# Kernel optimization log

Measured on AMD Instinct MI355X. Metric: run time of the kernel, lower is better.

## Reference

```python
import jax, jax.numpy as jnp
import numpy as np

B, N, E, EH, IB, DF, HID, P, TOPK, NE = 16, 978, 512, 512, 64, 2304, 512, 8, 50, 50000
SKIP = 0.2          # args.graph_skip_conn
NEG_INF = -1e20     # markoff value for non-top-k entries before softmax
LN_EPS = 1e-5


def setup_inputs() -> dict:
    key = jax.random.key(0)
    ks = jax.random.split(key, 20)
    g = lambda i, shape, s=0.05: jax.random.normal(ks[i], shape, dtype=jnp.float32) * s
    return dict(
        x1=jax.random.normal(ks[0], (B, N), dtype=jnp.float32),
        drug1=jax.random.normal(ks[1], (B, DF), dtype=jnp.float32),
        drug2=jax.random.normal(ks[2], (B, DF), dtype=jnp.float32),
        eps=jax.random.normal(ks[3], (B, IB), dtype=jnp.float32),
        edge_index=jax.random.randint(ks[4], (2, NE), 0, N),
        gate_W=g(5, (1, E)), gate_b=jnp.zeros((E,), jnp.float32),
        emb=g(6, (N, E), 1.0),
        encW1=g(7, (E, EH)), encb1=jnp.zeros((EH,), jnp.float32),
        encW2=g(8, (EH, 2 * IB)), encb2=jnp.zeros((2 * IB,), jnp.float32),
        netW1=g(9, (DF, E)), netb1=jnp.zeros((E,), jnp.float32),
        netW2=g(10, (E, 2 * IB)), netb2=jnp.zeros((2 * IB,), jnp.float32),
        ln_g=jnp.ones((2 * IB,), jnp.float32), ln_b=jnp.zeros((2 * IB,), jnp.float32),
        feat_mask=g(11, (4 * IB,), 1.0),
        W_sims=g(12, (P, 4 * IB, HID)),
        gcnW1=g(13, (2 * IB, HID)), gcnb1=jnp.zeros((HID,), jnp.float32),
        gcnW2=g(14, (HID, 2 * IB)), gcnb2=jnp.zeros((2 * IB,), jnp.float32),
        decW1=g(15, (IB, EH)), decb1=jnp.zeros((EH,), jnp.float32),
        bn_g=jnp.ones((EH,), jnp.float32), bn_b=jnp.zeros((EH,), jnp.float32),
        decW2=g(16, (EH, N)), decb2=jnp.zeros((N,), jnp.float32),
    )


def _forward(x1, drug1, drug2, eps, edge_index,
             gate_W, gate_b, emb, encW1, encb1, encW2, encb2,
             netW1, netb1, netW2, netb2, ln_g, ln_b,
             feat_mask, W_sims, gcnW1, gcnb1, gcnW2, gcnb2,
             decW1, decb1, bn_g, bn_b, decW2, decb2):
    # --- Encoder_x1: per-gene gated embedding -> MLP -> [B,N,2*IB] ---
    gate = jax.nn.sigmoid(x1[..., None] @ gate_W + gate_b)          # [B,N,E]
    h = gate * emb[None]                                            # [B,N,E]
    h = jax.nn.gelu(h @ encW1 + encb1, approximate=False)
    H = h @ encW2 + encb2                                           # [B,N,128]

    # --- drug feature net: Linear-ReLU-Linear-LayerNorm -> [B,128] ---
    def drug_embed(d):
        t = jax.nn.relu(d @ netW1 + netb1)
        t = t @ netW2 + netb2
        mu = t.mean(-1, keepdims=True)
        var = t.var(-1, keepdims=True)
        return (t - mu) * jax.lax.rsqrt(var + LN_EPS) * ln_g + ln_b

    D1 = drug_embed(drug1)
    D2 = drug_embed(drug2)
    fus1 = jnp.concatenate([H, jnp.broadcast_to(D1[:, None, :], (B, N, 2 * IB))], -1)  # [B,N,256]
    fus2 = jnp.concatenate([H, jnp.broadcast_to(D2[:, None, :], (B, N, 2 * IB))], -1)

    # --- init adjacency from edge_index (to_dense_adj), shared across batch ---
    init_adj = jnp.zeros((N, N), jnp.float32).at[edge_index[0], edge_index[1]].set(1.0)

    # --- attention-metric graph learner with feature denoise + kNN sparsify ---
    def learn_adj(fus):
        feats = fus * jax.nn.sigmoid(feat_mask)                      # feature mask
        hp = jax.nn.relu(jnp.einsum('bnd,pdh->bpnh', feats, W_sims)) # [B,P,N,HID]
        att = jnp.einsum('bpnh,bpmh->bnm', hp, hp) / P               # [B,N,N] (mean over perspectives)

        def sparsify(a):  # per-sample kNN mask + row softmax
            vals, idx = jax.lax.top_k(a, TOPK)
            out = jnp.full_like(a, NEG_INF).at[jnp.arange(N)[:, None], idx].set(vals)
            return jax.nn.softmax(out, axis=-1)

        adj = jax.vmap(sparsify)(att)
        return SKIP * init_adj[None] + (1.0 - SKIP) * adj

    adj1 = learn_adj(fus1)
    adj2 = learn_adj(fus2)

    # --- 2-layer GCN on learned graph (symmetric norm, self loops, edge weights) ---
    eye = jnp.eye(N, dtype=jnp.float32)

    def gcn_layer(x, adj, W, b):
        ahat = adj + eye[None]
        deg = ahat.sum(-2)                                           # in-degree by target (PyG flow)
        dinv = jax.lax.rsqrt(deg)
        norm = ahat * dinv[:, :, None] * dinv[:, None, :]            # [B,N,N]
        return jnp.einsum('bji,bjf->bif', norm, x @ W) + b

    t = jax.nn.relu(gcn_layer(H, adj1, gcnW1, gcnb1))
    node = gcn_layer(t, adj1, gcnW2, gcnb2)                          # [B,N,128]

    # --- global mean pool + VIB reparametrization ---
    gemb = node.mean(1)                                              # [B,128]
    mu = gemb[:, :IB]
    std = jax.nn.softplus(gemb[:, IB:] - IB)
    z = mu + eps * std                                               # [B,64]

    # --- decoder_x2: Linear-BatchNorm-ReLU-Linear-ReLU ---
    d = z @ decW1 + decb1
    bm = d.mean(0)
    bv = d.var(0)
    d = (d - bm) * jax.lax.rsqrt(bv + LN_EPS) * bn_g + bn_b
    d = jax.nn.relu(d)
    x2_pred = jax.nn.relu(d @ decW2 + decb2)                         # [B,N]
    return x2_pred, adj2, mu, std


def reference(x1, drug1, drug2, eps, edge_index,
              gate_W, gate_b, emb, encW1, encb1, encW2, encb2,
              netW1, netb1, netW2, netb2, ln_g, ln_b,
              feat_mask, W_sims, gcnW1, gcnb1, gcnW2, gcnb2,
              decW1, decb1, bn_g, bn_b, decW2, decb2):
    return _forward(x1, drug1, drug2, eps, edge_index,
                    gate_W, gate_b, emb, encW1, encb1, encW2, encb2,
                    netW1, netb1, netW2, netb2, ln_g, ln_b,
                    feat_mask, W_sims, gcnW1, gcnb1, gcnW2, gcnb2,
                    decW1, decb1, bn_g, bn_b, decW2, decb2)
```

## Files before the change

kernel.cpp:

```cpp
#include <hip/hip_runtime.h>
#include <cmath>

namespace {

constexpr int B = 16;
constexpr int N = 978;
constexpr int M = B * N;
constexpr int IB2 = 128;
constexpr int KATT = 4096;
constexpr int KCH = 1024;
constexpr int NCH = KATT / KCH;
constexpr int DF = 2304;
constexpr int TOPKK = 50;
constexpr int NEDGE = 50000;
constexpr int CANDMAX = 64;
constexpr int WST = 120;
constexpr int JQ = 245;

typedef __attribute__((ext_vector_type(8))) short bf16x8;
typedef __attribute__((ext_vector_type(4))) float f32x4;

__device__ __forceinline__ float geluf(float x) {
  return 0.5f * x * (1.f + erff(x * 0.7071067811865476f));
}
__device__ __forceinline__ float sigm(float x) { return 1.f / (1.f + expf(-x)); }
__device__ __forceinline__ double sigm64(double x) { return 1.0 / (1.0 + exp(-x)); }

__device__ __forceinline__ unsigned short f2bf(float f) {
  union { float f; unsigned u; } x; x.f = f;
  unsigned r = (x.u + 0x7FFFu + ((x.u >> 16) & 1u)) >> 16;
  return (unsigned short)r;
}
__device__ __forceinline__ float bf2f(unsigned short s) {
  union { float f; unsigned u; } x; x.u = ((unsigned)s) << 16; return x.f;
}

__global__ void k_wt(const float* __restrict__ wsims, const float* __restrict__ fm,
                     unsigned short* __restrict__ wth, unsigned short* __restrict__ wtl) {
  int t = blockIdx.x * 256 + threadIdx.x;
  int n = t >> 8, k = t & 255;
  int p = n >> 9, h = n & 511;
  double v = (double)wsims[(size_t)p * 131072 + (size_t)k * 512 + h] * sigm64((double)fm[k]);
  float vf = (float)v;
  unsigned short hi = f2bf(vf);
  wth[t] = hi;
  wtl[t] = f2bf(vf - bf2f(hi));
}

__global__ void k_wtrans(const float* __restrict__ W, unsigned short* __restrict__ TH,
                         unsigned short* __restrict__ TL, int K, int Nc) {
  int t = blockIdx.x * 256 + threadIdx.x;
  if (t >= K * Nc) return;
  int n = t / K, k = t - n * K;
  float v = W[(size_t)k * Nc + n];
  unsigned short hi = f2bf(v);
  TH[t] = hi;
  TL[t] = f2bf(v - bf2f(hi));
}

__global__ void k_fus(const float* __restrict__ Hb, const float* __restrict__ DD,
                      unsigned short* __restrict__ fh, unsigned short* __restrict__ fl) {
  int t = blockIdx.x * 256 + threadIdx.x;
  int k = t & 255;
  int row = t >> 8;
  int b = row / N;
  float v = (k < 128) ? Hb[(size_t)row * 128 + k] : DD[(size_t)b * 128 + (k - 128)];
  unsigned short hi = f2bf(v);
  fh[t] = hi;
  fl[t] = f2bf(v - bf2f(hi));
}

__global__ void k_gate_emb_bf(const float* __restrict__ x1, const float* __restrict__ gW,
                              const float* __restrict__ gb, const float* __restrict__ emb,
                              unsigned short* __restrict__ GH, unsigned short* __restrict__ GL) {
  size_t t = (size_t)blockIdx.x * 256 + threadIdx.x;
  int e = (int)(t & 511);
  size_t bn = t >> 9;
  int n = (int)(bn % N);
  float g = sigm(x1[bn] * gW[e] + gb[e]);
  float v = g * emb[(size_t)n * 512 + e];
  unsigned short hi = f2bf(v);
  GH[t] = hi;
  GL[t] = f2bf(v - bf2f(hi));
}

__global__ void k_zero(float* __restrict__ p, int n) {
  int t = blockIdx.x * 256 + threadIdx.x;
  if (t < n) p[t] = 0.f;
}

__global__ void k_scatter(const int* __restrict__ ei, float* __restrict__ adj) {
  int t = blockIdx.x * 256 + threadIdx.x;
  if (t < NEDGE) {
    int r = ei[t], c = ei[NEDGE + t];
    adj[(size_t)r * N + c] = 1.f;
  }
}

__device__ __forceinline__ void stage_tile(const unsigned short* __restrict__ gbase, int grow0,
                                           int rowmax, int k0, int ldk, char* lds, int tid) {
#pragma unroll
  for (int it = 0; it < 2; it++) {
    int r = (tid >> 2) + it * 64;
    int c8 = tid & 3;
    int gr = grow0 + r;
    uint4 v = make_uint4(0u, 0u, 0u, 0u);
    if (gr < rowmax) v = *reinterpret_cast<const uint4*>(&gbase[(size_t)gr * ldk + k0 + c8 * 8]);
    int off = (r * 64 + c8 * 16) ^ ((r & 7) << 4);
    *reinterpret_cast<uint4*>(lds + off) = v;
  }
}

__device__ __forceinline__ bf16x8 frag(const char* lds, int r, int k8) {
  int off = (r * 64 + k8 * 16) ^ ((r & 7) << 4);
  return *reinterpret_cast<const bf16x8*>(lds + off);
}

template <int ACT, bool HASBIAS, bool OUTF32, bool OUTBF>
__global__ __launch_bounds__(256) void k_mgemm(const unsigned short* __restrict__ AH,
                                               const unsigned short* __restrict__ AL,
                                               const unsigned short* __restrict__ BTH,
                                               const unsigned short* __restrict__ BTL,
                                               const float* __restrict__ bias,
                                               float* __restrict__ Cf,
                                               unsigned short* __restrict__ CbH,
                                               unsigned short* __restrict__ CbL,
                                               int Mm, int K, int Nc) {
  __shared__ __align__(16) char Ah[8192];
  __shared__ __align__(16) char Al[8192];
  __shared__ __align__(16) char Bh[8192];
  __shared__ __align__(16) char Bl[8192];
  const int m0 = blockIdx.x * 128;
  const int n0 = blockIdx.y * 128;
  const int tid = threadIdx.x;
  const int wave = tid >> 6, lane = tid & 63;
  f32x4 acc[2][8];
#pragma unroll
  for (int i = 0; i < 2; i++)
#pragma unroll
    for (int j = 0; j < 8; j++) acc[i][j] = (f32x4){0.f, 0.f, 0.f, 0.f};

  for (int k0 = 0; k0 < K; k0 += 32) {
    stage_tile(AH, m0, Mm, k0, K, Ah, tid);
    stage_tile(AL, m0, Mm, k0, K, Al, tid);
    stage_tile(BTH, n0, Nc, k0, K, Bh, tid);
    stage_tile(BTL, n0, Nc, k0, K, Bl, tid);
    __syncthreads();
    bf16x8 ah[2], al[2];
#pragma unroll
    for (int rf = 0; rf < 2; rf++) {
      int r = wave * 32 + rf * 16 + (lane & 15);
      ah[rf] = frag(Ah, r, lane >> 4);
      al[rf] = frag(Al, r, lane >> 4);
    }
#pragma unroll
    for (int cf = 0; cf < 8; cf++) {
      int rB = cf * 16 + (lane & 15);
      bf16x8 bh = frag(Bh, rB, lane >> 4);
      bf16x8 bl = frag(Bl, rB, lane >> 4);
#pragma unroll
      for (int rf = 0; rf < 2; rf++) {
        acc[rf][cf] = __builtin_amdgcn_mfma_f32_16x16x32_bf16(ah[rf], bh, acc[rf][cf], 0, 0, 0);
        acc[rf][cf] = __builtin_amdgcn_mfma_f32_16x16x32_bf16(ah[rf], bl, acc[rf][cf], 0, 0, 0);
        acc[rf][cf] = __builtin_amdgcn_mfma_f32_16x16x32_bf16(al[rf], bh, acc[rf][cf], 0, 0, 0);
      }
    }
    __syncthreads();
  }
#pragma unroll
  for (int rf = 0; rf < 2; rf++)
#pragma unroll
    for (int cf = 0; cf < 8; cf++)
#pragma unroll
      for (int r4 = 0; r4 < 4; r4++) {
        int row = m0 + wave * 32 + rf * 16 + ((lane >> 4) << 2) + r4;
        int col = n0 + cf * 16 + (lane & 15);
        if (row < Mm) {
          float v = acc[rf][cf][r4];
          if (HASBIAS) v += bias[col];
          if (ACT == 1) v = geluf(v);
          if (ACT == 2) v = fmaxf(v, 0.f);
          size_t idx = (size_t)row * Nc + col;
          if (OUTF32) Cf[idx] = v;
          if (OUTBF) {
            unsigned short hi = f2bf(v);
            CbH[idx] = hi;
            CbL[idx] = f2bf(v - bf2f(hi));
          }
        }
      }
}

__global__ __launch_bounds__(256) void k_hp_mma(const unsigned short* __restrict__ FH,
                                                const unsigned short* __restrict__ FL,
                                                const unsigned short* __restrict__ WTHc,
                                                const unsigned short* __restrict__ WTLc,
                                                float* __restrict__ CH) {
  __shared__ __align__(16) char Ah[8192];
  __shared__ __align__(16) char Al[8192];
  __shared__ __align__(16) char Bh[8192];
  __shared__ __align__(16) char Bl[8192];
  const int m0 = blockIdx.x * 128;
  const int n0 = blockIdx.y * 128;
  const int tid = threadIdx.x;
  const int wave = tid >> 6, lane = tid & 63;
  f32x4 acc[2][8];
#pragma unroll
  for (int i = 0; i < 2; i++)
#pragma unroll
    for (int j = 0; j < 8; j++) acc[i][j] = (f32x4){0.f, 0.f, 0.f, 0.f};

  for (int k0 = 0; k0 < 256; k0 += 32) {
    stage_tile(FH, m0, M, k0, 256, Ah, tid);
    stage_tile(FL, m0, M, k0, 256, Al, tid);
    stage_tile(WTHc, n0, KCH, k0, 256, Bh, tid);
    stage_tile(WTLc, n0, KCH, k0, 256, Bl, tid);
    __syncthreads();
    bf16x8 ah[2], al[2];
#pragma unroll
    for (int rf = 0; rf < 2; rf++) {
      int r = wave * 32 + rf * 16 + (lane & 15);
      ah[rf] = frag(Ah, r, lane >> 4);
      al[rf] = frag(Al, r, lane >> 4);
    }
#pragma unroll
    for (int cf = 0; cf < 8; cf++) {
      int rB = cf * 16 + (lane & 15);
      bf16x8 bh = frag(Bh, rB, lane >> 4);
      bf16x8 bl = frag(Bl, rB, lane >> 4);
#pragma unroll
      for (int rf = 0; rf < 2; rf++) {
        acc[rf][cf] = __builtin_amdgcn_mfma_f32_16x16x32_bf16(ah[rf], bh, acc[rf][cf], 0, 0, 0);
        acc[rf][cf] = __builtin_amdgcn_mfma_f32_16x16x32_bf16(ah[rf], bl, acc[rf][cf], 0, 0, 0);
        acc[rf][cf] = __builtin_amdgcn_mfma_f32_16x16x32_bf16(al[rf], bh, acc[rf][cf], 0, 0, 0);
      }
    }
    __syncthreads();
  }
#pragma unroll
  for (int rf = 0; rf < 2; rf++)
#pragma unroll
    for (int cf = 0; cf < 8; cf++)
#pragma unroll
      for (int r4 = 0; r4 < 4; r4++) {
        int row = m0 + wave * 32 + rf * 16 + ((lane >> 4) << 2) + r4;
        int col = n0 + cf * 16 + (lane & 15);
        if (row < M) CH[(size_t)row * KCH + col] = fmaxf(acc[rf][cf][r4], 0.f);
      }
}

__global__ __launch_bounds__(256) void k_mu(const float* __restrict__ CH, float* __restrict__ MU) {
  __shared__ double red[8][33];
  int b = blockIdx.y, jg = blockIdx.x;
  int jloc = threadIdx.x & 31, s = threadIdx.x >> 5;
  int j = jg * 32 + jloc;
  const float* p = CH + (size_t)b * N * KCH + j;
  double acc = 0.0;
  for (int n = s; n < N; n += 8) acc += (double)p[(size_t)n * KCH];
  red[s][jloc] = acc;
  __syncthreads();
  if (s == 0) {
    double t = 0.0;
#pragma unroll
    for (int k = 0; k < 8; k++) t += red[k][jloc];
    MU[b * KCH + j] = (float)(t * (1.0 / (double)N));
  }
}

__global__ __launch_bounds__(256) void k_centerq(const float* __restrict__ CH,
                                                 const float* __restrict__ MU,
                                                 unsigned short* __restrict__ CHB,
                                                 double* __restrict__ qv) {
  int r = blockIdx.x * 4 + (threadIdx.x >> 6);
  int lane = threadIdx.x & 63;
  int b = r / N;
  const float* row = CH + (size_t)r * KCH;
  const float* mu = MU + (size_t)b * KCH;
  double q = 0.0;
#pragma unroll
  for (int jp = 0; jp < 2; jp++) {
    int j0 = lane * 8 + jp * 512;
    float4 v0 = *reinterpret_cast<const float4*>(&row[j0]);
    float4 v1 = *reinterpret_cast<const float4*>(&row[j0 + 4]);
    float4 m0 = *reinterpret_cast<const float4*>(&mu[j0]);
    float4 m1 = *reinterpret_cast<const float4*>(&mu[j0 + 4]);
    unsigned short cb[8];
    cb[0] = f2bf(v0.x - m0.x); cb[1] = f2bf(v0.y - m0.y);
    cb[2] = f2bf(v0.z - m0.z); cb[3] = f2bf(v0.w - m0.w);
    cb[4] = f2bf(v1.x - m1.x); cb[5] = f2bf(v1.y - m1.y);
    cb[6] = f2bf(v1.z - m1.z); cb[7] = f2bf(v1.w - m1.w);
    *reinterpret_cast<uint4*>(&CHB[(size_t)r * KCH + j0]) = *reinterpret_cast<uint4*>(cb);
    q += (double)m0.x * v0.x + (double)m0.y * v0.y + (double)m0.z * v0.z + (double)m0.w * v0.w
       + (double)m1.x * v1.x + (double)m1.y * v1.y + (double)m1.z * v1.z + (double)m1.w * v1.w;
  }
  for (int off = 32; off > 0; off >>= 1) q += __shfl_down(q, off);
  if (lane == 0) qv[r] += q;
}

template <bool ACC>
__global__ __launch_bounds__(256) void k_syrk_mma(const unsigned short* __restrict__ CHB,
                                                  float* __restrict__ ATT) {
  __shared__ __align__(16) char At[8192];
  __shared__ __align__(16) char Bt[8192];
  const int T = 8;
  int pr = blockIdx.x;
  int ti = 0, rem = pr;
  while (rem >= T - ti) { rem -= T - ti; ti++; }
  int tj = ti + rem;
  int b = blockIdx.y;
  const unsigned short* base = CHB + (size_t)b * N * KCH;
  const int tid = threadIdx.x;
  const int wave = tid >> 6, lane = tid & 63;
  f32x4 acc[2][8];
#pragma unroll
  for (int i = 0; i < 2; i++)
#pragma unroll
    for (int j = 0; j < 8; j++) acc[i][j] = (f32x4){0.f, 0.f, 0.f, 0.f};

  for (int k0 = 0; k0 < KCH; k0 += 32) {
    stage_tile(base, ti * 128, N, k0, KCH, At, tid);
    stage_tile(base, tj * 128, N, k0, KCH, Bt, tid);
    __syncthreads();
    bf16x8 af[2];
#pragma unroll
    for (int rf = 0; rf < 2; rf++)
      af[rf] = frag(At, wave * 32 + rf * 16 + (lane & 15), lane >> 4);
#pragma unroll
    for (int cf = 0; cf < 8; cf++) {
      bf16x8 bf_ = frag(Bt, cf * 16 + (lane & 15), lane >> 4);
#pragma unroll
      for (int rf = 0; rf < 2; rf++)
        acc[rf][cf] = __builtin_amdgcn_mfma_f32_16x16x32_bf16(af[rf], bf_, acc[rf][cf], 0, 0, 0);
    }
    __syncthreads();
  }
  float* att = ATT + (size_t)b * N * N;
#pragma unroll
  for (int rf = 0; rf < 2; rf++)
#pragma unroll
    for (int cf = 0; cf < 8; cf++)
#pragma unroll
      for (int r4 = 0; r4 < 4; r4++) {
        int row = ti * 128 + wave * 32 + rf * 16 + ((lane >> 4) << 2) + r4;
        int col = tj * 128 + cf * 16 + (lane & 15);
        if (row < N && col < N) {
          float v = acc[rf][cf][r4];
          if (ACC) {
            att[(size_t)row * N + col] += v;
            if (ti != tj) att[(size_t)col * N + row] += v;
          } else {
            att[(size_t)row * N + col] = v;
            if (ti != tj) att[(size_t)col * N + row] = v;
          }
        }
      }
}

__global__ __launch_bounds__(256) void k_topk(float* __restrict__ ATT, const double* __restrict__ qv,
                                              const float* __restrict__ INITA,
                                              int* __restrict__ fcnt, int* __restrict__ frow,
                                              int* __restrict__ fcw, int* __restrict__ fidx,
                                              float* __restrict__ fv32) {
  int row = blockIdx.x;
  int n = row % N;
  int b = row / N;
  float* arow = ATT + (size_t)row * N;
  __shared__ unsigned keys[1024];
  __shared__ float svs[1024];
  __shared__ float outr[N];
  __shared__ float sred;
  __shared__ int s_slot, s_cw;
  int tid = threadIdx.x;
  double qn = qv[row];
  unsigned kreg[4];
#pragma unroll
  for (int c = 0; c < 4; c++) {
    int i = tid + 256 * c;
    unsigned kk = 0xFFFFFFFFu;
    float sv = -1e30f;
    if (i < N) {
      sv = (float)((double)arow[i] + qv[(size_t)b * N + i] - qn);
      unsigned u = __float_as_uint(sv);
      u ^= (u >> 31) ? 0xFFFFFFFFu : 0x80000000u;
      kk = ((~u) & 0xFFFFFC00u) | (unsigned)i;
    }
    svs[i] = sv;
    kreg[c] = kk;
  }
  __syncthreads();
  for (int ksz = 2; ksz <= 1024; ksz <<= 1) {
    for (int j = ksz >> 1; j > 0; j >>= 1) {
      if (j <= 32) {
#pragma unroll
        for (int c = 0; c < 4; c++) {
          int e = tid + 256 * c;
          unsigned pk = __shfl_xor(kreg[c], j);
          bool takemin = (((e & j) == 0) == ((e & ksz) == 0));
          unsigned mn = kreg[c] < pk ? kreg[c] : pk;
          unsigned mx = kreg[c] < pk ? pk : kreg[c];
          kreg[c] = takemin ? mn : mx;
        }
      } else if (j >= 256) {
        int sw = j >> 8;
#pragma unroll
        for (int c = 0; c < 4; c++) {
          if ((c & sw) == 0) {
            int e = tid + 256 * c;
            bool up = (e & ksz) == 0;
            unsigned a = kreg[c], b2 = kreg[c | sw];
            if ((a > b2) == up) { kreg[c] = b2; kreg[c | sw] = a; }
          }
        }
      } else {
#pragma unroll
        for (int c = 0; c < 4; c++) keys[tid + 256 * c] = kreg[c];
        __syncthreads();
#pragma unroll
        for (int c = 0; c < 4; c++) {
          int e = tid + 256 * c;
          unsigned pk = keys[e ^ j];
          bool takemin = (((e & j) == 0) == ((e & ksz) == 0));
          unsigned mn = kreg[c] < pk ? kreg[c] : pk;
          unsigned mx = kreg[c] < pk ? pk : kreg[c];
          kreg[c] = takemin ? mn : mx;
        }
        __syncthreads();
      }
    }
  }
#pragma unroll
  for (int c = 0; c < 4; c++) keys[tid + 256 * c] = kreg[c];
  __syncthreads();

  float v49 = svs[keys[49] & 1023u];
  float v50v = svs[keys[50] & 1023u];
  float FLAGW = 8e-3f + 2e-5f * fabsf(v49);
  bool flag = (v50v >= v49 - FLAGW);
  if (flag) {
    if (tid == 0) {
      int cin = 0;
      for (int r = 0; r < 50; r++)
        if (svs[keys[r] & 1023u] > v49 + FLAGW) cin++;
      int rhi = 50;
      while (rhi < 113) {
        float vv = svs[keys[rhi + 1] & 1023u];
        if (vv >= v49 - FLAGW) rhi++; else break;
      }
      int w = rhi - cin + 1;
      if (w > CANDMAX) w = CANDMAX;
      if (cin + w < 50) w = 50 - cin;
      int slot = atomicAdd(fcnt, 1);
      frow[slot] = row;
      fcw[slot] = cin | (w << 8);
      s_slot = slot;
      s_cw = cin | (w << 8);
    }
    __syncthreads();
    int slot = s_slot;
    int tot = (s_cw & 255) + (s_cw >> 8);
    for (int r = tid; r < tot; r += 256) {
      unsigned kk = keys[r];
      fidx[(size_t)slot * WST + r] = (int)(kk & 1023u);
      fv32[(size_t)slot * WST + r] = svs[kk & 1023u];
    }
    __syncthreads();
  }

  float vmax = svs[keys[0] & 1023u];
  float e = 0.f;
  int myidx = 0;
  if (tid < TOPKK) {
    unsigned kk = keys[tid];
    myidx = (int)(kk & 1023u);
    e = expf((svs[myidx] - vmax) * 0.125f);
  }
  float s = e;
  for (int off = 32; off > 0; off >>= 1) s += __shfl_down(s, off);
  if (tid == 0) sred = s;
  for (int m2 = tid; m2 < N; m2 += 256) outr[m2] = 0.2f * INITA[(size_t)n * N + m2];
  __syncthreads();
  if (tid < TOPKK) outr[myidx] = 0.2f * INITA[(size_t)n * N + myidx] + 0.8f * (e / sred);
  __syncthreads();
  for (int m2 = tid; m2 < N; m2 += 256) arow[m2] = outr[m2];
}

__global__ __launch_bounds__(256) void k_fixup(float* __restrict__ ATT, const float* __restrict__ INITA,
                                               const int* __restrict__ fcnt, const int* __restrict__ frow,
                                               const int* __restrict__ fcw, const int* __restrict__ fidx,
                                               const float* __restrict__ fv32) {
  __shared__ double wts[56];
  __shared__ int mm[56];
  __shared__ int s_tot;
  int tid = threadIdx.x;
  int cnt = *fcnt;
  for (int slot = blockIdx.x; slot < cnt; slot += gridDim.x) {
    int row = frow[slot];
    int cw = fcw[slot];
    int cin = cw & 255, w = cw >> 8;
    int n = row % N;
    __syncthreads();
    if (tid == 0) {
      int need = 50 - cin;
      if (need > w) need = w;
      double cv[CANDMAX]; int cm[CANDMAX]; float cs[CANDMAX];
      for (int c = 0; c < w; c++) {
        float sv = fv32[(size_t)slot * WST + cin + c];
        cv[c] = (double)sv * 0.125;
        cm[c] = fidx[(size_t)slot * WST + cin + c];
        cs[c] = sv;
      }
      int ord[CANDMAX];
      for (int c = 0; c < w; c++) ord[c] = c;
      for (int a2 = 0; a2 < w; a2++) {
        int best = a2;
        for (int c2 = a2 + 1; c2 < w; c2++) {
          int i1 = ord[c2], i0 = ord[best];
          if (cv[i1] > cv[i0] || (cv[i1] == cv[i0] && cm[i1] < cm[i0])) best = c2;
        }
        int tswap = ord[a2]; ord[a2] = ord[best]; ord[best] = tswap;
      }
      double b_in = cv[ord[need - 1]];
      double b_out = (need < w) ? cv[ord[need]] : -1e300;
      const double DATT = 1e-3;
      double fac[56];
      int tot = 0;
      for (int r = 0; r < cin; r++) {
        wts[tot] = (double)fv32[(size_t)slot * WST + r];
        mm[tot] = fidx[(size_t)slot * WST + r];
        fac[tot++] = 1.0;
      }
      if (need == w || b_in - b_out > DATT) {
        for (int t3 = 0; t3 < need; t3++) {
          wts[tot] = (double)cs[ord[t3]];
          mm[tot] = cm[ord[t3]];
          fac[tot++] = 1.0;
        }
      } else {
        int gs = 0;
        while (gs < w && cv[ord[gs]] > b_in + DATT) gs++;
        int ge = w - 1;
        while (ge >= 0 && cv[ord[ge]] < b_out - DATT) ge--;
        double mid = 0.5 * (b_in + b_out);
        while (ge - gs + 1 > 3) {
          if (cv[ord[gs]] - mid >= mid - cv[ord[ge]]) gs++;
          else ge--;
        }
        int fullc = gs;
        int gcount = ge - gs + 1;
        int gneed = need - fullc;
        if (gneed < 0) gneed = 0;
        if (gneed > gcount) gneed = gcount;
        double frac = (gcount > 0) ? (double)gneed / (double)gcount : 0.0;
        for (int t3 = 0; t3 < fullc; t3++) {
          wts[tot] = (double)cs[ord[t3]];
          mm[tot] = cm[ord[t3]];
          fac[tot++] = 1.0;
        }
        for (int t3 = gs; t3 <= ge; t3++) {
          wts[tot] = (double)cs[ord[t3]];
          mm[tot] = cm[ord[t3]];
          fac[tot++] = frac;
        }
      }
      double vmax = -1e300;
      for (int r = 0; r < tot; r++)
        if (fac[r] > 0.0 && wts[r] > vmax) vmax = wts[r];
      double S = 0.0;
      for (int r = 0; r < tot; r++) {
        double e = fac[r] * exp((wts[r] - vmax) * 0.125);
        wts[r] = e;
        S += e;
      }
      double inv = 1.0 / S;
      for (int r = 0; r < tot; r++) wts[r] *= inv;
      s_tot = tot;
    }
    __syncthreads();
    int tot = s_tot;
    float* arow = ATT + (size_t)row * N;
    for (int m2 = tid; m2 < N; m2 += 256) arow[m2] = 0.2f * INITA[(size_t)n * N + m2];
    __syncthreads();
    if (tid < tot && wts[tid] > 0.0)
      arow[mm[tid]] = 0.2f * INITA[(size_t)n * N + mm[tid]] + 0.8f * (float)wts[tid];
    __syncthreads();
  }
}

__global__ __launch_bounds__(256) void k_degp(const float* __restrict__ ADJ, float* __restrict__ DPART) {
  int ch = blockIdx.x, b = blockIdx.y;
  int tid = threadIdx.x;
  float reg[4] = {0.f, 0.f, 0.f, 0.f};
  int j0 = ch * 123, j1 = j0 + 123;
  if (j1 > N) j1 = N;
  const float* adj = ADJ + (size_t)b * N * N;
  for (int j = j0; j < j1; j++) {
    const float* rowp = adj + (size_t)j * N;
#pragma unroll
    for (int k = 0; k < 4; k++) {
      int i = tid + 256 * k;
      if (i < N) reg[k] += rowp[i];
    }
  }
  float* dp = DPART + ((size_t)b * 8 + ch) * N;
#pragma unroll
  for (int k = 0; k < 4; k++) {
    int i = tid + 256 * k;
    if (i < N) dp[i] = reg[k];
  }
}
__global__ void k_degf(const float* __restrict__ DPART, float* __restrict__ DINV) {
  int t = blockIdx.x * 256 + threadIdx.x;
  if (t >= M) return;
  int b = t / N, i = t - b * N;
  float s = 1.f;
#pragma unroll
  for (int c = 0; c < 8; c++) s += DPART[((size_t)b * 8 + c) * N + i];
  DINV[t] = rsqrtf(s);
}

__global__ __launch_bounds__(256) void k_spmmp(const float* __restrict__ ADJ, const float* __restrict__ DINV,
                                               const float* __restrict__ X, float* __restrict__ PP) {
  __shared__ float As[16][132];
  __shared__ float Ws[16][132];
  const int tid = threadIdx.x;
  const int i0 = blockIdx.x * 128;
  const int b = blockIdx.z >> 2;
  const int q = blockIdx.z & 3;
  const int jstart = q * JQ;
  const int jend = (q == 3) ? N : (jstart + JQ);
  const float* adj = ADJ + (size_t)b * N * N;
  const float* dv = DINV + b * N;
  const float* xb = X + (size_t)b * N * 128;
  const int ty = tid >> 4, tx = tid & 15;
  float acc[8][8];
#pragma unroll
  for (int i = 0; i < 8; i++)
#pragma unroll
    for (int j = 0; j < 8; j++) acc[i][j] = 0.f;

  for (int j0 = jstart; j0 < jend; j0 += 16) {
#pragma unroll
    for (int l = 0; l < 8; l++) {
      int idx = tid + l * 256;
      int r = idx >> 7, c = idx & 127;
      int j = j0 + r, i = i0 + c;
      float v = 0.f;
      if (j < jend && i < N) {
        float dj = dv[j];
        v = adj[(size_t)j * N + i] * dj;
        if (i == j) v += dj;
      }
      As[r][c] = v;
      float w = 0.f;
      if (j < jend) w = xb[(size_t)j * 128 + c];
      Ws[r][c] = w;
    }
    __syncthreads();
#pragma unroll
    for (int k = 0; k < 16; k++) {
      float a[8], bb[8];
      *reinterpret_cast<float4*>(&a[0]) = *reinterpret_cast<const float4*>(&As[k][ty * 8]);
      *reinterpret_cast<float4*>(&a[4]) = *reinterpret_cast<const float4*>(&As[k][ty * 8 + 4]);
      *reinterpret_cast<float4*>(&bb[0]) = *reinterpret_cast<const float4*>(&Ws[k][tx * 8]);
      *reinterpret_cast<float4*>(&bb[4]) = *reinterpret_cast<const float4*>(&Ws[k][tx * 8 + 4]);
#pragma unroll
      for (int i = 0; i < 8; i++)
#pragma unroll
        for (int j = 0; j < 8; j++) acc[i][j] = fmaf(a[i], bb[j], acc[i][j]);
    }
    __syncthreads();
  }
#pragma unroll
  for (int i = 0; i < 8; i++) {
    int row = i0 + ty * 8 + i;
    if (row >= N) continue;
#pragma unroll
    for (int j4 = 0; j4 < 2; j4++) {
      float4 v;
      float* vv = reinterpret_cast<float*>(&v);
#pragma unroll
      for (int j = 0; j < 4; j++) vv[j] = acc[i][j4 * 4 + j];
      *reinterpret_cast<float4*>(&PP[(((size_t)q * M) + (size_t)b * N + row) * 128 +
                                     tx * 8 + j4 * 4]) = v;
    }
  }
}

template <bool HASBIAS, bool OUTBF>
__global__ void k_spmmc(const float* __restrict__ PP, const float* __restrict__ DINV,
                        const float* __restrict__ bias, float* __restrict__ OUT,
                        unsigned short* __restrict__ OH, unsigned short* __restrict__ OL) {
  int t = blockIdx.x * 256 + threadIdx.x;
  int row = t >> 7, f = t & 127;
  float v = ((PP[t] + PP[(size_t)M * 128 + t]) +
             (PP[(size_t)2 * M * 128 + t] + PP[(size_t)3 * M * 128 + t])) * DINV[row];
  if (HASBIAS) v += bias[f];
  if (OUTBF) {
    unsigned short hi = f2bf(v);
    OH[t] = hi;
    OL[t] = f2bf(v - bf2f(hi));
  } else {
    OUT[t] = v;
  }
}

__global__ __launch_bounds__(256) void k_drug_l1(const float* __restrict__ d1, const float* __restrict__ d2,
                                                 const float* __restrict__ W, const float* __restrict__ bias,
                                                 float* __restrict__ T1) {
  __shared__ float row[DF];
  int blk = blockIdx.x;
  const float* dr = ((blk & 16) ? d2 : d1) + (size_t)(blk & 15) * DF;
  for (int i = threadIdx.x; i < DF; i += 256) row[i] = dr[i];
  __syncthreads();
  for (int e = threadIdx.x; e < 512; e += 256) {
    float s = bias[e];
    for (int k = 0; k < DF; k++) s = fmaf(row[k], W[(size_t)k * 512 + e], s);
    T1[(size_t)blk * 512 + e] = fmaxf(s, 0.f);
  }
}

__global__ __launch_bounds__(128) void k_drug_l2(const float* __restrict__ T1, const float* __restrict__ W,
                                                 const float* __restrict__ bias, const float* __restrict__ lg,
                                                 const float* __restrict__ lb, float* __restrict__ D) {
  __shared__ float row[512];
  __shared__ float red[4];
  int blk = blockIdx.x;
  int e = threadIdx.x;
  for (int i = e; i < 512; i += 128) row[i] = T1[(size_t)blk * 512 + i];
  __syncthreads();
  float s = bias[e];
  for (int k = 0; k < 512; k++) s = fmaf(row[k], W[k * 128 + e], s);
  float t = s;
  for (int off = 32; off > 0; off >>= 1) t += __shfl_down(t, off);
  if ((e & 63) == 0) red[e >> 6] = t;
  __syncthreads();
  float mean = (red[0] + red[1]) * (1.f / 128.f);
  float dd = s - mean;
  float wv = dd * dd;
  for (int off = 32; off > 0; off >>= 1) wv += __shfl_down(wv, off);
  if ((e & 63) == 0) red[2 + (e >> 6)] = wv;
  __syncthreads();
  float var = (red[2] + red[3]) * (1.f / 128.f);
  D[(size_t)blk * 128 + e] = dd * rsqrtf(var + 1e-5f) * lg[e] + lb[e];
}

__global__ void k_gemb(const float* __restrict__ NODE, float* __restrict__ GEMB) {
  int t = blockIdx.x * 256 + threadIdx.x;
  int b = t >> 7, f = t & 127;
  const float* p = NODE + (size_t)b * N * IB2 + f;
  float s = 0.f;
  for (int n2 = 0; n2 < N; n2++) s += p[(size_t)n2 * IB2];
  GEMB[t] = s * (1.f / (float)N);
}

__global__ void k_heads(const float* __restrict__ GEMB, const float* __restrict__ EPS,
                        float* __restrict__ out_mu, float* __restrict__ out_std, float* __restrict__ Z) {
  int t = blockIdx.x * 256 + threadIdx.x;
  int b = t >> 6, q = t & 63;
  float mu = GEMB[b * 128 + q];
  float xs = GEMB[b * 128 + 64 + q] - 64.f;
  float sp = (xs > 20.f) ? xs : log1pf(expf(xs));
  out_mu[t] = mu;
  out_std[t] = sp;
  Z[t] = mu + EPS[t] * sp;
}

__global__ __launch_bounds__(512) void k_dec1(const float* __restrict__ Z, const float* __restrict__ W1,
                                              const float* __restrict__ b1, const float* __restrict__ bg,
                                              const float* __restrict__ bb, float* __restrict__ DEC) {
  int f = threadIdx.x;
  float d[16];
  for (int b = 0; b < 16; b++) {
    float s = b1[f];
    for (int k = 0; k < 64; k++) s = fmaf(Z[b * 64 + k], W1[k * 512 + f], s);
    d[b] = s;
  }
  float m = 0.f;
  for (int b = 0; b < 16; b++) m += d[b];
  m *= (1.f / 16.f);
  float v = 0.f;
  for (int b = 0; b < 16; b++) { float t = d[b] - m; v += t * t; }
  v *= (1.f / 16.f);
  float sc = rsqrtf(v + 1e-5f) * bg[f];
  float sh = bb[f];
  for (int b = 0; b < 16; b++) {
    float x = (d[b] - m) * sc + sh;
    DEC[b * 512 + f] = fmaxf(x, 0.f);
  }
}

__global__ void k_dec2(const float* __restrict__ DEC, const float* __restrict__ W2,
                       const float* __restrict__ b2, float* __restrict__ X2) {
  int t = blockIdx.x * 256 + threadIdx.x;
  if (t >= M) return;
  int b = t / N, n2 = t - b * N;
  float s = b2[n2];
  const float* db = DEC + b * 512;
  for (int f = 0; f < 512; f++) s = fmaf(db[f], W2[(size_t)f * N + n2], s);
  X2[t] = fmaxf(s, 0.f);
}

}

extern "C" void kernel_launch(void* const* d_in, const int* in_sizes, int n_in,
                              void* d_out, int out_size, void* d_ws, size_t ws_size,
                              hipStream_t stream) {
  const float* x1 = (const float*)d_in[0];
  const float* drug1 = (const float*)d_in[1];
  const float* drug2 = (const float*)d_in[2];
  const float* eps = (const float*)d_in[3];
  const int* ei = (const int*)d_in[4];
  const float* gate_W = (const float*)d_in[5];
  const float* gate_b = (const float*)d_in[6];
  const float* emb = (const float*)d_in[7];
  const float* encW1 = (const float*)d_in[8];
  const float* encb1 = (const float*)d_in[9];
  const float* encW2 = (const float*)d_in[10];
  const float* encb2 = (const float*)d_in[11];
  const float* netW1 = (const float*)d_in[12];
  const float* netb1 = (const float*)d_in[13];
  const float* netW2 = (const float*)d_in[14];
  const float* netb2 = (const float*)d_in[15];
  const float* ln_g = (const float*)d_in[16];
  const float* ln_b = (const float*)d_in[17];
  const float* feat_mask = (const float*)d_in[18];
  const float* W_sims = (const float*)d_in[19];
  const float* gcnW1 = (const float*)d_in[20];
  const float* gcnb1 = (const float*)d_in[21];
  const float* gcnW2 = (const float*)d_in[22];
  const float* gcnb2 = (const float*)d_in[23];
  const float* decW1 = (const float*)d_in[24];
  const float* decb1 = (const float*)d_in[25];
  const float* bn_g = (const float*)d_in[26];
  const float* bn_b = (const float*)d_in[27];
  const float* decW2 = (const float*)d_in[28];
  const float* decb2 = (const float*)d_in[29];
  (void)in_sizes; (void)n_in; (void)out_size; (void)ws_size;

  size_t o = 0;
  auto A = [&](size_t bytes) { char* p = (char*)d_ws + o; o += (bytes + 255) & ~(size_t)255; return p; };
  unsigned short* WTH = (unsigned short*)A((size_t)KATT * 256 * 2);
  unsigned short* WTL = (unsigned short*)A((size_t)KATT * 256 * 2);
  char* RBIG = A((size_t)64 * 1024 * 1024);
  float* Hb = (float*)A((size_t)M * 128 * 4);
  float* ADJ1 = (float*)A((size_t)B * N * N * 4);
  float* INITA = (float*)A((size_t)N * N * 4);
  float* T1 = (float*)A(32 * 512 * 4);
  float* Dd32 = (float*)A(32 * 128 * 4);
  float* DINV = (float*)A(M * 4);
  float* DPART = (float*)A((size_t)16 * 8 * N * 4);
  float* GEMB = (float*)A(B * 128 * 4);
  float* Zb = (float*)A(B * 64 * 4);
  float* DEC = (float*)A(B * 512 * 4);
  int* fcnt = (int*)A(256);
  float* MU = (float*)A((size_t)B * KCH * 4);
  double* qv = (double*)A((size_t)M * 8);
  unsigned short* FUSH = (unsigned short*)A((size_t)M * 256 * 2);
  unsigned short* FUSL = (unsigned short*)A((size_t)M * 256 * 2);
  unsigned short* CHB = (unsigned short*)A((size_t)M * KCH * 2);
  unsigned short* WE1H = (unsigned short*)A(512 * 512 * 2);
  unsigned short* WE1L = (unsigned short*)A(512 * 512 * 2);
  unsigned short* WE2H = (unsigned short*)A(128 * 512 * 2);
  unsigned short* WE2L = (unsigned short*)A(128 * 512 * 2);
  unsigned short* WG1H = (unsigned short*)A(512 * 128 * 2);
  unsigned short* WG1L = (unsigned short*)A(512 * 128 * 2);
  unsigned short* WG2H = (unsigned short*)A(128 * 512 * 2);
  unsigned short* WG2L = (unsigned short*)A(128 * 512 * 2);

  unsigned short* GEH = (unsigned short*)RBIG;
  unsigned short* GEL = (unsigned short*)(RBIG + (size_t)16 * 1024 * 1024);
  unsigned short* H1H = (unsigned short*)(RBIG + (size_t)32 * 1024 * 1024);
  unsigned short* H1L = (unsigned short*)(RBIG + (size_t)48 * 1024 * 1024);
  float* CH = (float*)RBIG;
  char* FLAGS = RBIG;
  int* frow = (int*)FLAGS;
  int* fcw = (int*)(FLAGS + (size_t)M * 4);
  int* fidx = (int*)(FLAGS + (size_t)2 * M * 4);
  float* fv32 = (float*)(FLAGS + (size_t)2 * M * 4 + (size_t)M * WST * 4);
  unsigned short* AGGH = (unsigned short*)RBIG;
  unsigned short* AGGL = (unsigned short*)(RBIG + (size_t)4 * 1024 * 1024);
  float* PP = (float*)(RBIG + (size_t)8 * 1024 * 1024);
  unsigned short* TTH = CHB;
  unsigned short* TTL = CHB + (size_t)M * 512;
  float* TW2 = (float*)FUSH;
  float* NODE = (float*)FUSL;

  float* out = (float*)d_out;
  float* out_x2 = out;
  float* out_adj2 = out + M;
  float* out_mu = out + M + (size_t)B * N * N;
  float* out_std = out_mu + B * 64;

  k_wt<<<4096, 256, 0, stream>>>(W_sims, feat_mask, WTH, WTL);
  k_wtrans<<<1024, 256, 0, stream>>>(encW1, WE1H, WE1L, 512, 512);
  k_wtrans<<<256, 256, 0, stream>>>(encW2, WE2H, WE2L, 512, 128);
  k_wtrans<<<256, 256, 0, stream>>>(gcnW1, WG1H, WG1L, 128, 512);
  k_wtrans<<<256, 256, 0, stream>>>(gcnW2, WG2H, WG2L, 512, 128);
  k_gate_emb_bf<<<31296, 256, 0, stream>>>(x1, gate_W, gate_b, emb, GEH, GEL);
  k_mgemm<1, true, false, true><<<dim3(123, 4), 256, 0, stream>>>(
      GEH, GEL, WE1H, WE1L, encb1, nullptr, H1H, H1L, M, 512, 512);
  k_mgemm<0, true, true, false><<<dim3(123, 1), 256, 0, stream>>>(
      H1H, H1L, WE2H, WE2L, encb2, Hb, nullptr, nullptr, M, 512, 128);
  k_drug_l1<<<32, 256, 0, stream>>>(drug1, drug2, netW1, netb1, T1);
  k_drug_l2<<<32, 128, 0, stream>>>(T1, netW2, netb2, ln_g, ln_b, Dd32);
  k_zero<<<(N * N + 255) / 256, 256, 0, stream>>>(INITA, N * N);
  k_scatter<<<(NEDGE + 255) / 256, 256, 0, stream>>>(ei, INITA);

  for (int g = 0; g < 2; g++) {
    float* att = (g == 0) ? ADJ1 : out_adj2;
    const float* DDg = Dd32 + (size_t)g * 16 * 128;
    hipMemsetAsync(fcnt, 0, 4, stream);
    hipMemsetAsync(qv, 0, (size_t)M * 8, stream);
    k_fus<<<15648, 256, 0, stream>>>(Hb, DDg, FUSH, FUSL);
    for (int c = 0; c < NCH; c++) {
      k_hp_mma<<<dim3(123, KCH / 128), 256, 0, stream>>>(FUSH, FUSL, WTH + (size_t)c * KCH * 256,
                                                         WTL + (size_t)c * KCH * 256, CH);
      k_mu<<<dim3(KCH / 32, 16), 256, 0, stream>>>(CH, MU);
      k_centerq<<<M / 4, 256, 0, stream>>>(CH, MU, CHB, qv);
      if (c == 0)
        k_syrk_mma<false><<<dim3(36, 16), 256, 0, stream>>>(CHB, att);
      else
        k_syrk_mma<true><<<dim3(36, 16), 256, 0, stream>>>(CHB, att);
    }
    k_topk<<<M, 256, 0, stream>>>(att, qv, INITA, fcnt, frow, fcw, fidx, fv32);
    k_fixup<<<1024, 256, 0, stream>>>(att, INITA, fcnt, frow, fcw, fidx, fv32);
  }

  k_degp<<<dim3(8, 16), 256, 0, stream>>>(ADJ1, DPART);
  k_degf<<<(M + 255) / 256, 256, 0, stream>>>(DPART, DINV);
  k_spmmp<<<dim3(8, 1, 64), 256, 0, stream>>>(ADJ1, DINV, Hb, PP);
  k_spmmc<false, true><<<(M * 128) / 256, 256, 0, stream>>>(PP, DINV, nullptr, nullptr, AGGH, AGGL);
  k_mgemm<2, true, false, true><<<dim3(123, 4), 256, 0, stream>>>(
      AGGH, AGGL, WG1H, WG1L, gcnb1, nullptr, TTH, TTL, M, 128, 512);
  k_mgemm<0, false, true, false><<<dim3(123, 1), 256, 0, stream>>>(
      TTH, TTL, WG2H, WG2L, nullptr, TW2, nullptr, nullptr, M, 512, 128);
  k_spmmp<<<dim3(8, 1, 64), 256, 0, stream>>>(ADJ1, DINV, TW2, PP);
  k_spmmc<true, false><<<(M * 128) / 256, 256, 0, stream>>>(PP, DINV, gcnb2, NODE, nullptr, nullptr);
  k_gemb<<<8, 256, 0, stream>>>(NODE, GEMB);
  k_heads<<<4, 256, 0, stream>>>(GEMB, eps, out_mu, out_std, Zb);
  k_dec1<<<1, 512, 0, stream>>>(Zb, decW1, decb1, bn_g, bn_b, DEC);
  k_dec2<<<(M + 255) / 256, 256, 0, stream>>>(DEC, decW2, decb2, out_x2);
}
```

Measured before the change: 3.236 ms.

## Replace full bitonic sort in top-k with radix select plus small sort

The per-row top-k kernel now runs a 4-pass 8-bit radix histogram select to find the 128th smallest key. It compacts the keys at or below that threshold into a 128-entry buffer and bitonic-sorts only those, instead of sorting all 1024 keys. Separately, the graph-mean reduction is split into a 128-block partial-sum kernel and a final reduce, replacing an 8-block serial loop. The aim is to cut sort work and barriers in the launch-heavy top-k kernel and to expose more parallelism in the mean, at the cost of shared-memory atomics, serial histogram scans by one thread, and an extra launch.

```diff
diff --git a/kernel.cpp b/kernel.cpp
--- a/kernel.cpp
+++ b/kernel.cpp
@@ -365,8 +365,12 @@
   int n = row % N;
   int b = row / N;
   float* arow = ATT + (size_t)row * N;
-  __shared__ unsigned keys[1024];
   __shared__ float svs[1024];
+  __shared__ int hist[256];
+  __shared__ unsigned s_pref;
+  __shared__ int s_need;
+  __shared__ unsigned cand[128];
+  __shared__ int cctr;
   __shared__ float outr[N];
   __shared__ float sred;
   __shared__ int s_slot, s_cw;
@@ -387,63 +391,79 @@
     svs[i] = sv;
     kreg[c] = kk;
   }
+  if (tid == 0) { s_pref = 0u; s_need = 128; }
+  for (int lvl = 0; lvl < 4; lvl++) {
+    int shift = 24 - 8 * lvl;
+    hist[tid] = 0;
+    __syncthreads();
+    unsigned himask = (lvl == 0) ? 0u : (0xFFFFFFFFu << (shift + 8));
+    unsigned pref = s_pref;
+#pragma unroll
+    for (int c = 0; c < 4; c++) {
+      unsigned k = kreg[c];
+      if ((k & himask) == pref) atomicAdd(&hist[(k >> shift) & 255u], 1);
+    }
+    __syncthreads();
+    if (tid == 0) {
+      int nd = s_need, cum = 0;
+      for (int t2 = 0; t2 < 256; t2++) {
+        int h = hist[t2];
+        if (cum + h >= nd) { s_pref |= ((unsigned)t2 << shift); s_need = nd - cum; break; }
+        cum += h;
+      }
+    }
+    __syncthreads();
+  }
+  unsigned K128 = s_pref;
+  if (tid == 0) cctr = 0;
   __syncthreads();
-  for (int ksz = 2; ksz <= 1024; ksz <<= 1) {
+#pragma unroll
+  for (int c = 0; c < 4; c++) {
+    if (kreg[c] <= K128) {
+      int sl = atomicAdd(&cctr, 1);
+      cand[sl] = kreg[c];
+    }
+  }
+  __syncthreads();
+  unsigned myk = (tid < 128) ? cand[tid] : 0xFFFFFFFFu;
+  for (int ksz = 2; ksz <= 128; ksz <<= 1) {
     for (int j = ksz >> 1; j > 0; j >>= 1) {
-      if (j <= 32) {
-#pragma unroll
-        for (int c = 0; c < 4; c++) {
-          int e = tid + 256 * c;
-          unsigned pk = __shfl_xor(kreg[c], j);
-          bool takemin = (((e & j) == 0) == ((e & ksz) == 0));
-          unsigned mn = kreg[c] < pk ? kreg[c] : pk;
-          unsigned mx = kreg[c] < pk ? pk : kreg[c];
-          kreg[c] = takemin ? mn : mx;
-        }
-      } else if (j >= 256) {
-        int sw = j >> 8;
-#pragma unroll
-        for (int c = 0; c < 4; c++) {
-          if ((c & sw) == 0) {
-            int e = tid + 256 * c;
-            bool up = (e & ksz) == 0;
-            unsigned a = kreg[c], b2 = kreg[c | sw];
-            if ((a > b2) == up) { kreg[c] = b2; kreg[c | sw] = a; }
-          }
-        }
-      } else {
-#pragma unroll
-        for (int c = 0; c < 4; c++) keys[tid + 256 * c] = kreg[c];
+      if (j == 64) {
+        if (tid < 128) cand[tid] = myk;
         __syncthreads();
-#pragma unroll
-        for (int c = 0; c < 4; c++) {
-          int e = tid + 256 * c;
-          unsigned pk = keys[e ^ j];
-          bool takemin = (((e & j) == 0) == ((e & ksz) == 0));
-          unsigned mn = kreg[c] < pk ? kreg[c] : pk;
-          unsigned mx = kreg[c] < pk ? pk : kreg[c];
-          kreg[c] = takemin ? mn : mx;
+        if (tid < 128) {
+          unsigned pk = cand[tid ^ 64];
+          bool takemin = (((tid & 64) == 0) == ((tid & ksz) == 0));
+          unsigned mn = myk < pk ? myk : pk;
+          unsigned mx = myk < pk ? pk : myk;
+          myk = takemin ? mn : mx;
         }
         __syncthreads();
-      }
-    }
-  }
-#pragma unroll
-  for (int c = 0; c < 4; c++) keys[tid + 256 * c] = kreg[c];
+      } else {
+        unsigned pk = __shfl_xor(myk, j);
+        int e = tid & 127;
+        bool takemin = (((e & j) == 0) == ((e & ksz) == 0));
+        unsigned mn = myk < pk ? myk : pk;
+        unsigned mx = myk < pk ? pk : myk;
+        if (tid < 128) myk = takemin ? mn : mx;
+      }
+    }
+  }
+  if (tid < 128) cand[tid] = myk;
   __syncthreads();
 
-  float v49 = svs[keys[49] & 1023u];
-  float v50v = svs[keys[50] & 1023u];
+  float v49 = svs[cand[49] & 1023u];
+  float v50v = svs[cand[50] & 1023u];
   float FLAGW = 8e-3f + 2e-5f * fabsf(v49);
   bool flag = (v50v >= v49 - FLAGW);
   if (flag) {
     if (tid == 0) {
       int cin = 0;
       for (int r = 0; r < 50; r++)
-        if (svs[keys[r] & 1023u] > v49 + FLAGW) cin++;
+        if (svs[cand[r] & 1023u] > v49 + FLAGW) cin++;
       int rhi = 50;
       while (rhi < 113) {
-        float vv = svs[keys[rhi + 1] & 1023u];
+        float vv = svs[cand[rhi + 1] & 1023u];
         if (vv >= v49 - FLAGW) rhi++; else break;
       }
       int w = rhi - cin + 1;
@@ -459,18 +479,18 @@
     int slot = s_slot;
     int tot = (s_cw & 255) + (s_cw >> 8);
     for (int r = tid; r < tot; r += 256) {
-      unsigned kk = keys[r];
+      unsigned kk = cand[r];
       fidx[(size_t)slot * WST + r] = (int)(kk & 1023u);
       fv32[(size_t)slot * WST + r] = svs[kk & 1023u];
     }
     __syncthreads();
   }
 
-  float vmax = svs[keys[0] & 1023u];
+  float vmax = svs[cand[0] & 1023u];
   float e = 0.f;
   int myidx = 0;
   if (tid < TOPKK) {
-    unsigned kk = keys[tid];
+    unsigned kk = cand[tid];
     myidx = (int)(kk & 1023u);
     e = expf((svs[myidx] - vmax) * 0.125f);
   }
@@ -744,12 +764,21 @@
   D[(size_t)blk * 128 + e] = dd * rsqrtf(var + 1e-5f) * lg[e] + lb[e];
 }
 
-__global__ void k_gemb(const float* __restrict__ NODE, float* __restrict__ GEMB) {
+__global__ __launch_bounds__(256) void k_gembp(const float* __restrict__ NODE, float* __restrict__ GP) {
+  int b = blockIdx.y;
+  int sp = blockIdx.x * 2 + (threadIdx.x >> 7);
+  int f = threadIdx.x & 127;
+  const float* p = NODE + (size_t)b * N * IB2 + f;
+  float s = 0.f;
+  for (int n2 = sp; n2 < N; n2 += 16) s += p[(size_t)n2 * IB2];
+  GP[((size_t)b * 16 + sp) * 128 + f] = s;
+}
+__global__ void k_gembf(const float* __restrict__ GP, float* __restrict__ GEMB) {
   int t = blockIdx.x * 256 + threadIdx.x;
   int b = t >> 7, f = t & 127;
-  const float* p = NODE + (size_t)b * N * IB2 + f;
   float s = 0.f;
-  for (int n2 = 0; n2 < N; n2++) s += p[(size_t)n2 * IB2];
+#pragma unroll
+  for (int k = 0; k < 16; k++) s += GP[((size_t)b * 16 + k) * 128 + f];
   GEMB[t] = s * (1.f / (float)N);
 }
 
@@ -850,6 +879,7 @@
   float* DINV = (float*)A(M * 4);
   float* DPART = (float*)A((size_t)16 * 8 * N * 4);
   float* GEMB = (float*)A(B * 128 * 4);
+  float* GP = (float*)A((size_t)B * 16 * 128 * 4);
   float* Zb = (float*)A(B * 64 * 4);
   float* DEC = (float*)A(B * 512 * 4);
   int* fcnt = (int*)A(256);
@@ -936,7 +966,8 @@
       TTH, TTL, WG2H, WG2L, nullptr, TW2, nullptr, nullptr, M, 512, 128);
   k_spmmp<<<dim3(8, 1, 64), 256, 0, stream>>>(ADJ1, DINV, TW2, PP);
   k_spmmc<true, false><<<(M * 128) / 256, 256, 0, stream>>>(PP, DINV, gcnb2, NODE, nullptr, nullptr);
-  k_gemb<<<8, 256, 0, stream>>>(NODE, GEMB);
+  k_gembp<<<dim3(8, 16), 256, 0, stream>>>(NODE, GP);
+  k_gembf<<<8, 256, 0, stream>>>(GP, GEMB);
   k_heads<<<4, 256, 0, stream>>>(GEMB, eps, out_mu, out_std, Zb);
   k_dec1<<<1, 512, 0, stream>>>(Zb, decW1, decb1, bn_g, bn_b, DEC);
   k_dec2<<<(M + 255) / 256, 256, 0, stream>>>(DEC, decW2, decb2, out_x2);
```

After: 3.696 ms. 14.2% more time.
